# Kernel tuning notes

Hardware: AMD Instinct MI355X
Metric: run time of the kernel (lower is better)

## Reference

```python
import jax, jax.numpy as jnp
import numpy as np
from jax import lax

B, N, G, K, ED = 16, 32768, 128, 64, 384
EPS = 1e-5


def setup_inputs() -> dict:
    key = jax.random.key(0)
    ks = jax.random.split(key, 8)
    def p(k, shape, scale=0.05):
        return jax.random.normal(k, shape, jnp.float32) * scale
    return dict(
        points=jax.random.normal(ks[0], (B, N, 3), jnp.float32),
        w1=p(ks[1], (128, 3)), b1=jnp.zeros((128,), jnp.float32),
        bn1_g=jnp.ones((128,), jnp.float32), bn1_b=jnp.zeros((128,), jnp.float32),
        bn1_m=jnp.zeros((128,), jnp.float32), bn1_v=jnp.ones((128,), jnp.float32),
        w2=p(ks[2], (256, 128)), b2=jnp.zeros((256,), jnp.float32),
        w3=p(ks[3], (512, 512)), b3=jnp.zeros((512,), jnp.float32),
        bn2_g=jnp.ones((512,), jnp.float32), bn2_b=jnp.zeros((512,), jnp.float32),
        bn2_m=jnp.zeros((512,), jnp.float32), bn2_v=jnp.ones((512,), jnp.float32),
        w4=p(ks[4], (ED, 512)), b4=jnp.zeros((ED,), jnp.float32),
    )


def _sq_cdist(a, b):
    # squared euclidean distances; same ordering as torch.cdist for argmin/topk
    return (jnp.sum(a * a, -1)[..., :, None]
            + jnp.sum(b * b, -1)[..., None, :]
            - 2.0 * jnp.einsum('...ic,...jc->...ij', a, b))


def _fps(points, num_samples):
    # farthest point sampling (deterministic start at index 0) -> [B, S] indices
    b, n, _ = points.shape
    def step(carry, _):
        dist, far = carry
        centroid = points[jnp.arange(b), far][:, None, :]        # [B,1,3]
        d = jnp.sum((points - centroid) ** 2, -1)                # [B,N]
        dist = jnp.minimum(dist, d)
        return (dist, jnp.argmax(dist, -1)), far
    init = (jnp.full((b, n), jnp.inf, points.dtype), jnp.zeros((b,), jnp.int32))
    _, idxs = lax.scan(step, init, None, length=num_samples)
    return idxs.T                                                 # [B,S]


def _morton_sort(center, g):
    # greedy nearest-neighbor ordering of centroids -> flat global indices [B*G]
    b = center.shape[0]
    idx_base = jnp.arange(b) * g
    d = _sq_cdist(center, center)                                 # [B,G,G]
    eye = jnp.eye(g, dtype=bool)
    d = jnp.where(eye[None], jnp.inf, d)
    dist_flat = d.reshape(b * g, g)
    def step(carry, _):
        df, cur = carry
        row = df[cur]                                             # [B,G]
        closest = jnp.argmin(row, -1) + idx_base                  # [B] global
        df = df.at[closest].set(jnp.inf)
        return (df, closest), closest
    (_, _), rest = lax.scan(step, (dist_flat, idx_base), None, length=g - 1)
    return jnp.concatenate([idx_base[None], rest], 0).T.reshape(-1)


def _bn(x, gamma, beta, mean, var):
    # eval-mode BatchNorm1d over channel axis of [BG, C, K]
    inv = gamma * lax.rsqrt(var + EPS)
    return x * inv[None, :, None] + (beta - mean * inv)[None, :, None]


def _encoder(pg, w1, b1, bn1_g, bn1_b, bn1_m, bn1_v, w2, b2,
             w3, b3, bn2_g, bn2_b, bn2_m, bn2_v, w4, b4):
    # pg: [B, G, K, 3] -> [B, G, ED]
    bs, g, k, _ = pg.shape
    x = pg.reshape(bs * g, k, 3)
    f = jnp.einsum('oi,bki->bok', w1, x) + b1[None, :, None]      # [BG,128,K]
    f = jax.nn.relu(_bn(f, bn1_g, bn1_b, bn1_m, bn1_v))
    f = jnp.einsum('oi,bik->bok', w2, f) + b2[None, :, None]      # [BG,256,K]
    fg = jnp.max(f, axis=2, keepdims=True)                        # [BG,256,1]
    f = jnp.concatenate([jnp.broadcast_to(fg, f.shape), f], 1)    # [BG,512,K]
    f = jnp.einsum('oi,bik->bok', w3, f) + b3[None, :, None]
    f = jax.nn.relu(_bn(f, bn2_g, bn2_b, bn2_m, bn2_v))
    f = jnp.einsum('oi,bik->bok', w4, f) + b4[None, :, None]      # [BG,ED,K]
    return jnp.max(f, axis=2).reshape(bs, g, ED)


def reference(points, w1, b1, bn1_g, bn1_b, bn1_m, bn1_v, w2, b2,
              w3, b3, bn2_g, bn2_b, bn2_m, bn2_v, w4, b4):
    b = points.shape[0]
    bidx = jnp.arange(b)
    cid = _fps(points, G)                                         # [B,G]
    centroids = points[bidx[:, None], cid]                        # [B,G,3]
    d = _sq_cdist(centroids, points)                              # [B,G,N]
    _, nbr_idx = lax.top_k(-d, K)                                 # [B,G,K] smallest
    neighbors = points[bidx[:, None, None], nbr_idx]              # [B,G,K,3]
    local = neighbors - centroids[:, :, None, :]
    sidx = _morton_sort(centroids, G)                             # [B*G]
    local = local.reshape(b * G, K, 3)[sidx].reshape(b, G, K, 3)
    centroids = centroids.reshape(b * G, 3)[sidx].reshape(b, G, 3)
    tokens = _encoder(local, w1, b1, bn1_g, bn1_b, bn1_m, bn1_v, w2, b2,
                      w3, b3, bn2_g, bn2_b, bn2_m, bn2_v, w4, b4)
    return centroids, tokens
```

## Files before the change

### kernel.cpp

```cpp
#include <hip/hip_runtime.h>
#include <math.h>

#define BB   16
#define NN   32768
#define GG   128
#define KK   64
#define EDD  384
#define NT1  1024
#define PPT  32
#define SB   16
#define SP   (NN / SB)
#define JP   (SP / NT1)

#define WS_GC     0
#define WS_F2     6240
#define WS_FG     530528
#define WS_F4     538720
#define WS_SYNC   1587296

#define GOFF_WSUM  (NN)
#define GOFF_CNT   (NN + 32)
#define GOFF_SEL   (NN + 40)
#define GOFF_EQB   (NN + 104)
#define GOFF_XL    (NN + 616)
#define GRP_LDS_FLOATS (NN + 808)

__device__ __forceinline__ float sq3(float a, float b, float c) {
  return __fadd_rn(__fadd_rn(__fmul_rn(a, a), __fmul_rn(b, b)), __fmul_rn(c, c));
}
__device__ __forceinline__ float dot3(float ax, float ay, float az,
                                      float bx, float by, float bz) {
  return __fadd_rn(__fadd_rn(__fmul_rn(ax, bx), __fmul_rn(ay, by)), __fmul_rn(az, bz));
}
__device__ __forceinline__ unsigned long long shfl_xor_u64(unsigned long long v,
                                                           int off) {
  unsigned lo = (unsigned)v, hi = (unsigned)(v >> 32);
  lo = __shfl_xor(lo, off);
  hi = __shfl_xor(hi, off);
  return ((unsigned long long)hi << 32) | lo;
}

__global__ void __launch_bounds__(NT1) k_fps(const float* __restrict__ points,
                                             float* __restrict__ out,
                                             float* __restrict__ ws) {
  __shared__ float2 xyS[SP];
  __shared__ float  zS[SP];
  __shared__ float cent[GG * 3];
  __shared__ float darr[GG];
  __shared__ int msh[1];
  __shared__ unsigned long long redp[2][16];
  __shared__ unsigned long long winp;

  const int gb   = blockIdx.x;
  const int b    = (gb & 7) * 2 + (gb >> 7);
  const int blk  = (gb >> 3) & 15;
  const int t    = threadIdx.x;
  const int wave = t >> 6, lane = t & 63;
  const float* P = points + (size_t)b * NN * 3;
  const int base = blk * SP;
  unsigned long long* slots = (unsigned long long*)(ws + WS_SYNC);

#pragma unroll
  for (int j = 0; j < JP; ++j) {
    int q = t + j * NT1;
    const float* pp = P + (size_t)(base + q) * 3;
    xyS[q] = make_float2(pp[0], pp[1]);
    zS[q]  = pp[2];
  }
  float dist[JP];
#pragma unroll
  for (int j = 0; j < JP; ++j) dist[j] = INFINITY;

  float cx = P[0], cy = P[1], cz = P[2];
  if (blk == 0 && t == 0) { cent[0] = cx; cent[1] = cy; cent[2] = cz; }
  if (t == 0) winp = 0ULL;
  __syncthreads();

  for (int it = 1; it < GG; ++it) {
    const int par = it & 1;
    float bd = -INFINITY; int bj = 0;
#pragma unroll
    for (int j = 0; j < JP; ++j) {
      int q = t + j * NT1;
      float2 xy = xyS[q];
      float  zz = zS[q];
      float dx = __fsub_rn(xy.x, cx);
      float dy = __fsub_rn(xy.y, cy);
      float dz = __fsub_rn(zz, cz);
      float d  = __fadd_rn(__fadd_rn(__fmul_rn(dx, dx), __fmul_rn(dy, dy)),
                           __fmul_rn(dz, dz));
      float nd = fminf(dist[j], d);
      dist[j] = nd;
      if (nd > bd) { bd = nd; bj = j; }
    }
    unsigned long long bp =
        ((unsigned long long)__float_as_uint(bd) << 32) |
        ((unsigned)it << 16) |
        (unsigned)(0xFFFF - (base + t + (bj << 10)));
#pragma unroll
    for (int off = 1; off < 64; off <<= 1) {
      unsigned long long o = shfl_xor_u64(bp, off);
      if (o > bp) bp = o;
    }
    if (lane == 0) redp[par][wave] = bp;
    __syncthreads();
    unsigned long long w;
    if (wave == 0) {
      unsigned long long v = redp[par][lane & 15];
#pragma unroll
      for (int off = 1; off < 16; off <<= 1) {
        unsigned long long o = shfl_xor_u64(v, off);
        if (o > v) v = o;
      }
      unsigned long long* sl = slots + ((size_t)par * 16 + b) * SB;
      if (lane == 0)
        __hip_atomic_store(&sl[blk], v, __ATOMIC_RELAXED,
                           __HIP_MEMORY_SCOPE_AGENT);
      if (lane < SB) {
        unsigned long long o;
        do {
          o = __hip_atomic_load(&sl[lane], __ATOMIC_RELAXED,
                                __HIP_MEMORY_SCOPE_AGENT);
        } while ((unsigned)((o >> 16) & 0xFFFF) != (unsigned)it);
        unsigned long long o1 = shfl_xor_u64(o, 1);
        if (o1 > o) o = o1;
        unsigned long long o2 = shfl_xor_u64(o, 2);
        if (o2 > o) o = o2;
        unsigned long long o4 = shfl_xor_u64(o, 4);
        if (o4 > o) o = o4;
        unsigned long long o8 = shfl_xor_u64(o, 8);
        if (o8 > o) o = o8;
        if (lane == 0)
          __hip_atomic_store(&winp, o, __ATOMIC_RELAXED,
                             __HIP_MEMORY_SCOPE_WORKGROUP);
        w = o;
      }
      w = shfl_xor_u64(w, 0);
      {
        unsigned lo = (unsigned)w, hi = (unsigned)(w >> 32);
        lo = __shfl(lo, 0);
        hi = __shfl(hi, 0);
        w = ((unsigned long long)hi << 32) | lo;
      }
    } else {
      do {
        w = __hip_atomic_load(&winp, __ATOMIC_RELAXED,
                              __HIP_MEMORY_SCOPE_WORKGROUP);
      } while ((unsigned)((w >> 16) & 0xFFFF) != (unsigned)it);
    }
    int sv = 0xFFFF - (int)(w & 0xFFFF);
    const float* wp = P + (size_t)sv * 3;
    cx = wp[0]; cy = wp[1]; cz = wp[2];
    if (blk == 0 && t == 0) {
      cent[it * 3 + 0] = cx; cent[it * 3 + 1] = cy; cent[it * 3 + 2] = cz;
    }
  }

  if (blk != 0) return;
  __syncthreads();

  if (t < GG) {
    float c0x = cent[0], c0y = cent[1], c0z = cent[2];
    float cjx = cent[t * 3 + 0], cjy = cent[t * 3 + 1], cjz = cent[t * 3 + 2];
    float sa = sq3(c0x, c0y, c0z);
    float sb = sq3(cjx, cjy, cjz);
    float dt = dot3(c0x, c0y, c0z, cjx, cjy, cjz);
    float dd = __fsub_rn(__fadd_rn(sa, sb), __fmul_rn(2.0f, dt));
    darr[t] = (t == 0) ? INFINITY : dd;
  }
  __syncthreads();
  if (t == 0) {
    float vd = darr[1]; int vi = 1;
    for (int j = 2; j < GG; ++j) {
      float od = darr[j];
      if (od < vd) { vd = od; vi = j; }
    }
    msh[0] = vi;
    float* gc = ws + WS_GC + b * 6;
    gc[0] = cent[0];          gc[1] = cent[1];          gc[2] = cent[2];
    gc[3] = cent[vi * 3 + 0]; gc[4] = cent[vi * 3 + 1]; gc[5] = cent[vi * 3 + 2];
  }
  __syncthreads();
  int m = msh[0];
  if (t < GG * 3) {
    int pos = t / 3, c = t % 3;
    float v = (pos == 1) ? cent[m * 3 + c] : cent[c];
    out[(size_t)b * GG * 3 + t] = v;
  }
}

__global__ void __launch_bounds__(NT1) k_grp(
    const float* __restrict__ points, float* __restrict__ ws,
    const float* __restrict__ w1, const float* __restrict__ b1,
    const float* __restrict__ g1, const float* __restrict__ be1,
    const float* __restrict__ m1, const float* __restrict__ v1,
    const float* __restrict__ w2, const float* __restrict__ b2) {
  extern __shared__ float smem[];
  unsigned* dkey = (unsigned*)smem;
  float* f1s  = smem;
  unsigned* wsum = (unsigned*)(smem + GOFF_WSUM);
  int*   cnts = (int*)(smem + GOFF_CNT);
  int*   sel  = (int*)(smem + GOFF_SEL);
  int*   eqb  = (int*)(smem + GOFF_EQB);
  float* xl   = smem + GOFF_XL;

  const int g = blockIdx.x;
  const int b = g >> 1, which = g & 1;
  const int t = threadIdx.x;
  const int wave = t >> 6, lane = t & 63;
  const float* P = points + (size_t)b * NN * 3;
  const float* gc = ws + WS_GC + b * 6 + which * 3;
  const float cx = gc[0], cy = gc[1], cz = gc[2];
  const float sa = sq3(cx, cy, cz);

#pragma unroll
  for (int j = 0; j < PPT; ++j) {
    int p = t + j * NT1;
    const float* pp = P + (size_t)p * 3;
    float px = pp[0], py = pp[1], pz = pp[2];
    float sb = sq3(px, py, pz);
    float dt = dot3(cx, cy, cz, px, py, pz);
    float d  = __fsub_rn(__fadd_rn(sa, sb), __fmul_rn(2.0f, dt));
    unsigned u = __float_as_uint(d);
    dkey[p] = u ^ ((u & 0x80000000u) ? 0xFFFFFFFFu : 0x80000000u);
  }
  if (t < 2) cnts[t] = 0;
  __syncthreads();

  unsigned klo = 0u, khi = 0xFFFFFFFFu;
  int par = 0;
  while (klo < khi) {
    unsigned mid = klo + ((khi - klo) >> 1);
    int c = 0;
#pragma unroll
    for (int j = 0; j < PPT; ++j) c += (dkey[t + j * NT1] <= mid) ? 1 : 0;
#pragma unroll
    for (int off = 1; off < 64; off <<= 1) c += __shfl_xor(c, off);
    if (lane == 0) wsum[par * 16 + wave] = (unsigned)c;
    __syncthreads();
    int tot = 0;
#pragma unroll
    for (int w = 0; w < 16; ++w) tot += (int)wsum[par * 16 + w];
    if (tot >= KK) khi = mid; else klo = mid + 1;
    par ^= 1;
  }
  const unsigned K64 = klo;

  {
    int c = 0;
#pragma unroll
    for (int j = 0; j < PPT; ++j) c += (dkey[t + j * NT1] < K64) ? 1 : 0;
#pragma unroll
    for (int off = 1; off < 64; off <<= 1) c += __shfl_xor(c, off);
    if (lane == 0) wsum[par * 16 + wave] = (unsigned)c;
    __syncthreads();
  }
  int C_lt = 0;
#pragma unroll
  for (int w = 0; w < 16; ++w) C_lt += (int)wsum[par * 16 + w];

#pragma unroll
  for (int j = 0; j < PPT; ++j) {
    int p = t + j * NT1;
    unsigned kk = dkey[p];
    if (kk < K64) {
      int pos = atomicAdd(&cnts[0], 1);
      sel[pos] = p;
    } else if (kk == K64) {
      int pos = atomicAdd(&cnts[1], 1);
      if (pos < 512) eqb[pos] = p;
    }
  }
  __syncthreads();

  if (wave == 0) {
    int M = cnts[1]; if (M > 512) M = 512;
    int R = KK - C_lt;
    int e[8];
#pragma unroll
    for (int q = 0; q < 8; ++q) {
      int ix = lane + q * 64;
      e[q] = (ix < M) ? eqb[ix] : 0x7FFFFFFF;
    }
    for (int r = 0; r < R; ++r) {
      int gm = e[0];
#pragma unroll
      for (int q = 1; q < 8; ++q) gm = min(gm, e[q]);
#pragma unroll
      for (int off = 1; off < 64; off <<= 1) gm = min(gm, __shfl_xor(gm, off));
      if (lane == 0) sel[C_lt + r] = gm;
#pragma unroll
      for (int q = 0; q < 8; ++q) if (e[q] == gm) e[q] = 0x7FFFFFFF;
    }
  }
  __syncthreads();

  if (t < KK) {
    int p = sel[t];
    const float* pp = P + (size_t)p * 3;
    xl[t * 3 + 0] = __fsub_rn(pp[0], cx);
    xl[t * 3 + 1] = __fsub_rn(pp[1], cy);
    xl[t * 3 + 2] = __fsub_rn(pp[2], cz);
  }
  __syncthreads();

  {
    const int o = t & 127, kh = t >> 7;
    float wx = w1[o * 3 + 0], wy = w1[o * 3 + 1], wz = w1[o * 3 + 2];
    float inv = g1[o] * (1.0f / sqrtf(v1[o] + 1e-5f));
    float add = be1[o] - m1[o] * inv;
    float bb = b1[o];
#pragma unroll
    for (int kk = 0; kk < 8; ++kk) {
      int k = kh * 8 + kk;
      float f = fmaf(wx, xl[k * 3 + 0],
                fmaf(wy, xl[k * 3 + 1],
                fmaf(wz, xl[k * 3 + 2], bb)));
      f = fmaf(f, inv, add);
      f1s[o * 65 + k] = fmaxf(f, 0.0f);
    }
  }
  __syncthreads();

  const int k  = t & 63;
  const int og = __builtin_amdgcn_readfirstlane(t >> 6);
  const int o0 = og * 16;
  float acc[16];
#pragma unroll
  for (int oo = 0; oo < 16; ++oo) acc[oo] = b2[o0 + oo];
  for (int i = 0; i < 128; ++i) {
    float xv = f1s[i * 65 + k];
#pragma unroll
    for (int oo = 0; oo < 16; ++oo)
      acc[oo] = fmaf(w2[(o0 + oo) * 128 + i], xv, acc[oo]);
  }
  float* f2g = ws + WS_F2 + (size_t)g * 256 * 64;
  float* fgg = ws + WS_FG + g * 256;
#pragma unroll
  for (int oo = 0; oo < 16; ++oo) f2g[(o0 + oo) * 64 + k] = acc[oo];
#pragma unroll
  for (int oo = 0; oo < 16; ++oo) {
    float v = acc[oo];
#pragma unroll
    for (int off = 1; off < 64; off <<= 1) v = fmaxf(v, __shfl_xor(v, off));
    if (k == 0) fgg[o0 + oo] = v;
  }
}

__global__ void __launch_bounds__(256) k_encB(
    float* __restrict__ ws,
    const float* __restrict__ w3, const float* __restrict__ b3,
    const float* __restrict__ g2, const float* __restrict__ be2,
    const float* __restrict__ m2, const float* __restrict__ v2) {
  __shared__ float part[32][8];
  __shared__ float sfg[32];
  const int blk = blockIdx.x;
  const int g = blk >> 4, oc = blk & 15;
  const int t = threadIdx.x;
  const int k = t & 63;
  const int og = __builtin_amdgcn_readfirstlane(t >> 6);
  const int ob = oc * 32;
  const float* fgg = ws + WS_FG + g * 256;
  {
    int o = t >> 3, ih = t & 7;
    float s = 0.0f;
    int i0 = ih * 32;
    for (int ii = 0; ii < 32; ++ii) {
      int i = i0 + ii;
      s = fmaf(w3[(size_t)(ob + o) * 512 + i], fgg[i], s);
    }
    part[o][ih] = s;
  }
  __syncthreads();
  if (t < 32) {
    float s = ((part[t][0] + part[t][1]) + (part[t][2] + part[t][3])) +
              ((part[t][4] + part[t][5]) + (part[t][6] + part[t][7]));
    sfg[t] = b3[ob + t] + s;
  }
  __syncthreads();
  const int o0 = ob + og * 8;
  float acc[8];
#pragma unroll
  for (int oo = 0; oo < 8; ++oo) acc[oo] = sfg[og * 8 + oo];
  const float* f2g = ws + WS_F2 + (size_t)g * 256 * 64;
#pragma unroll 4
  for (int i = 0; i < 256; ++i) {
    float xv = f2g[i * 64 + k];
#pragma unroll
    for (int oo = 0; oo < 8; ++oo)
      acc[oo] = fmaf(w3[(size_t)(o0 + oo) * 512 + 256 + i], xv, acc[oo]);
  }
  float* f4g = ws + WS_F4 + (size_t)g * 512 * 64;
#pragma unroll
  for (int oo = 0; oo < 8; ++oo) {
    int o = o0 + oo;
    float inv = g2[o] * (1.0f / sqrtf(v2[o] + 1e-5f));
    float add = be2[o] - m2[o] * inv;
    f4g[o * 64 + k] = fmaxf(fmaf(acc[oo], inv, add), 0.0f);
  }
}

__global__ void __launch_bounds__(256) k_encCb(float* __restrict__ ws,
                                               const float* __restrict__ w4,
                                               const float* __restrict__ b4,
                                               float* __restrict__ out) {
  const int blk = blockIdx.x;
  const int g = blk / 24, oc = blk % 24;
  const int b = g >> 1, which = g & 1;
  const int t = threadIdx.x;
  const int k = t & 63;
  const int og = __builtin_amdgcn_readfirstlane(t >> 6);
  const int o0 = oc * 16 + og * 4;
  float acc[4];
#pragma unroll
  for (int oo = 0; oo < 4; ++oo) acc[oo] = b4[o0 + oo];
  const float* f4g = ws + WS_F4 + (size_t)g * 512 * 64;
#pragma unroll 8
  for (int i = 0; i < 512; ++i) {
    float xv = f4g[i * 64 + k];
#pragma unroll
    for (int oo = 0; oo < 4; ++oo)
      acc[oo] = fmaf(w4[(size_t)(o0 + oo) * 512 + i], xv, acc[oo]);
  }
#pragma unroll
  for (int oo = 0; oo < 4; ++oo) {
#pragma unroll
    for (int off = 1; off < 64; off <<= 1)
      acc[oo] = fmaxf(acc[oo], __shfl_xor(acc[oo], off));
  }
  float* tok = out + (size_t)BB * GG * 3;
  if (which == 1) {
    if (k == 0) {
      float* dst = tok + ((size_t)b * GG + 1) * EDD + o0;
#pragma unroll
      for (int oo = 0; oo < 4; ++oo) dst[oo] = acc[oo];
    }
  } else {
#pragma unroll
    for (int rep = 0; rep < 2; ++rep) {
      int pos = k + rep * 64;
      if (pos == 1) continue;
      float* dst = tok + ((size_t)b * GG + pos) * EDD + o0;
#pragma unroll
      for (int oo = 0; oo < 4; ++oo) dst[oo] = acc[oo];
    }
  }
}

extern "C" void kernel_launch(void* const* d_in, const int* in_sizes, int n_in,
                              void* d_out, int out_size, void* d_ws, size_t ws_size,
                              hipStream_t stream) {
  const float* points = (const float*)d_in[0];
  const float* w1  = (const float*)d_in[1];
  const float* b1  = (const float*)d_in[2];
  const float* g1  = (const float*)d_in[3];
  const float* be1 = (const float*)d_in[4];
  const float* m1  = (const float*)d_in[5];
  const float* v1  = (const float*)d_in[6];
  const float* w2  = (const float*)d_in[7];
  const float* b2  = (const float*)d_in[8];
  const float* w3  = (const float*)d_in[9];
  const float* b3  = (const float*)d_in[10];
  const float* g2  = (const float*)d_in[11];
  const float* be2 = (const float*)d_in[12];
  const float* m2  = (const float*)d_in[13];
  const float* v2  = (const float*)d_in[14];
  const float* w4  = (const float*)d_in[15];
  const float* b4  = (const float*)d_in[16];
  float* out = (float*)d_out;
  float* ws  = (float*)d_ws;

  size_t dyn_grp = (size_t)GRP_LDS_FLOATS * sizeof(float);
  hipFuncSetAttribute(reinterpret_cast<const void*>(k_grp),
                      hipFuncAttributeMaxDynamicSharedMemorySize, (int)dyn_grp);

  hipMemsetAsync(ws + WS_SYNC, 0xAA, (size_t)2 * 16 * SB * 8, stream);

  hipLaunchKernelGGL(k_fps, dim3(BB * SB), dim3(NT1), 0, stream,
                     points, out, ws);
  hipLaunchKernelGGL(k_grp, dim3(32), dim3(NT1), dyn_grp, stream,
                     points, ws, w1, b1, g1, be1, m1, v1, w2, b2);
  hipLaunchKernelGGL(k_encB, dim3(512), dim3(256), 0, stream,
                     ws, w3, b3, g2, be2, m2, v2);
  hipLaunchKernelGGL(k_encCb, dim3(768), dim3(256), 0, stream, ws, w4, b4, out);
}
```

Measured before the change: 465.8 us.

## Replace bitwise binary search for k-th distance with 4-pass radix select

```diff
diff --git a/kernel.cpp b/kernel.cpp
--- a/kernel.cpp
+++ b/kernel.cpp
@@ -18,12 +18,13 @@
 #define WS_F4     538720
 #define WS_SYNC   1587296
 
-#define GOFF_WSUM  (NN)
-#define GOFF_CNT   (NN + 32)
-#define GOFF_SEL   (NN + 40)
-#define GOFF_EQB   (NN + 104)
-#define GOFF_XL    (NN + 616)
-#define GRP_LDS_FLOATS (NN + 808)
+#define GOFF_HIST  (NN)
+#define GOFF_HSUM  (NN + 4096)
+#define GOFF_CNT   (NN + 4352)
+#define GOFF_SEL   (NN + 4360)
+#define GOFF_EQB   (NN + 4424)
+#define GOFF_XL    (NN + 4936)
+#define GRP_LDS_FLOATS (NN + 5128)
 
 __device__ __forceinline__ float sq3(float a, float b, float c) {
   return __fadd_rn(__fadd_rn(__fmul_rn(a, a), __fmul_rn(b, b)), __fmul_rn(c, c));
@@ -135,7 +136,6 @@
                              __HIP_MEMORY_SCOPE_WORKGROUP);
         w = o;
       }
-      w = shfl_xor_u64(w, 0);
       {
         unsigned lo = (unsigned)w, hi = (unsigned)(w >> 32);
         lo = __shfl(lo, 0);
@@ -198,7 +198,8 @@
   extern __shared__ float smem[];
   unsigned* dkey = (unsigned*)smem;
   float* f1s  = smem;
-  unsigned* wsum = (unsigned*)(smem + GOFF_WSUM);
+  unsigned* histw = (unsigned*)(smem + GOFF_HIST);
+  unsigned* hsum  = (unsigned*)(smem + GOFF_HSUM);
   int*   cnts = (int*)(smem + GOFF_CNT);
   int*   sel  = (int*)(smem + GOFF_SEL);
   int*   eqb  = (int*)(smem + GOFF_EQB);
@@ -227,37 +228,59 @@
   if (t < 2) cnts[t] = 0;
   __syncthreads();
 
-  unsigned klo = 0u, khi = 0xFFFFFFFFu;
-  int par = 0;
-  while (klo < khi) {
-    unsigned mid = klo + ((khi - klo) >> 1);
-    int c = 0;
-#pragma unroll
-    for (int j = 0; j < PPT; ++j) c += (dkey[t + j * NT1] <= mid) ? 1 : 0;
-#pragma unroll
-    for (int off = 1; off < 64; off <<= 1) c += __shfl_xor(c, off);
-    if (lane == 0) wsum[par * 16 + wave] = (unsigned)c;
+  unsigned prefix = 0u;
+  int cnt_before = 0;
+#pragma unroll
+  for (int dpass = 0; dpass < 4; ++dpass) {
+    const int s = 24 - 8 * dpass;
+#pragma unroll
+    for (int i = 0; i < 4; ++i) histw[t + i * NT1] = 0u;
     __syncthreads();
-    int tot = 0;
-#pragma unroll
-    for (int w = 0; w < 16; ++w) tot += (int)wsum[par * 16 + w];
-    if (tot >= KK) khi = mid; else klo = mid + 1;
-    par ^= 1;
-  }
-  const unsigned K64 = klo;
-
-  {
-    int c = 0;
-#pragma unroll
-    for (int j = 0; j < PPT; ++j) c += (dkey[t + j * NT1] < K64) ? 1 : 0;
-#pragma unroll
-    for (int off = 1; off < 64; off <<= 1) c += __shfl_xor(c, off);
-    if (lane == 0) wsum[par * 16 + wave] = (unsigned)c;
+    unsigned* myh = histw + wave * 256;
+#pragma unroll
+    for (int j = 0; j < PPT; ++j) {
+      unsigned key = dkey[t + j * NT1];
+      bool match = (dpass == 0) || (((key ^ prefix) >> (s + 8)) == 0u);
+      if (match) atomicAdd(&myh[(key >> s) & 0xFFu], 1u);
+    }
     __syncthreads();
-  }
-  int C_lt = 0;
-#pragma unroll
-  for (int w = 0; w < 16; ++w) C_lt += (int)wsum[par * 16 + w];
+    if (t < 256) {
+      unsigned c = 0;
+#pragma unroll
+      for (int w = 0; w < 16; ++w) c += histw[w * 256 + t];
+      hsum[t] = c;
+    }
+    __syncthreads();
+    if (wave == 0) {
+      unsigned c0 = hsum[lane * 4 + 0], c1 = hsum[lane * 4 + 1];
+      unsigned c2 = hsum[lane * 4 + 2], c3 = hsum[lane * 4 + 3];
+      unsigned lsum = c0 + c1 + c2 + c3;
+      unsigned inc = lsum;
+#pragma unroll
+      for (int off = 1; off < 64; off <<= 1) {
+        unsigned o = __shfl_up(inc, off);
+        if (lane >= off) inc += o;
+      }
+      unsigned excl = inc - lsum;
+      int T = KK - cnt_before;
+      if ((int)excl < T && (int)(excl + lsum) >= T) {
+        unsigned cum = excl;
+        int B;
+        if ((int)(cum + c0) >= T) { B = lane * 4 + 0; }
+        else if ((int)(cum + c0 + c1) >= T) { B = lane * 4 + 1; cum += c0; }
+        else if ((int)(cum + c0 + c1 + c2) >= T) { B = lane * 4 + 2; cum += c0 + c1; }
+        else { B = lane * 4 + 3; cum += c0 + c1 + c2; }
+        cnts[2] = B;
+        cnts[3] = cnt_before + (int)cum;
+      }
+    }
+    __syncthreads();
+    prefix |= ((unsigned)cnts[2]) << s;
+    cnt_before = cnts[3];
+    __syncthreads();
+  }
+  const unsigned K64 = prefix;
+  const int C_lt = cnt_before;
 
 #pragma unroll
   for (int j = 0; j < PPT; ++j) {
```

New measurement: 451.9 us (median of 2 runs). 3.0% less time.
